# Kernel tuning notes

Hardware: AMD Instinct MI355X
Metric: run time of the kernel (lower is better)

The kernel has to match this reference:

```python
import jax, jax.numpy as jnp
import numpy as np

B, L, D, H = 1024, 128, 768, 256
EPS = 1e-5  # torch BatchNorm1d default eps


def _masked_mean(x, lens):
    # x: [B, L, D], lens: [B] int -> mean over first lens[i] rows per sample
    mask = (jnp.arange(x.shape[1])[None, :] < lens[:, None]).astype(x.dtype)  # [B, L]
    return jnp.einsum('bld,bl->bd', x, mask) / lens[:, None].astype(x.dtype)


def _batchnorm_train(x, gamma, beta):
    # training-mode BN: batch mean and biased variance
    mu = jnp.mean(x, axis=0)
    var = jnp.mean((x - mu) ** 2, axis=0)
    return gamma * (x - mu) / jnp.sqrt(var + EPS) + beta


def setup_inputs() -> dict:
    key = jax.random.key(0)
    ks = jax.random.split(key, 12)
    user_features = jax.random.normal(ks[0], (B, L, D), jnp.float32)
    hashtag_features = jax.random.normal(ks[1], (B, L, D), jnp.float32)
    user_lens = jax.random.randint(ks[2], (B,), 1, L + 1, jnp.int32)
    hashtag_lens = jax.random.randint(ks[3], (B,), 1, L + 1, jnp.int32)
    def lin(k, fan_out, fan_in):
        bound = 1.0 / np.sqrt(fan_in)
        kw, kb = jax.random.split(k)
        w = jax.random.uniform(kw, (fan_out, fan_in), jnp.float32, -bound, bound)
        b = jax.random.uniform(kb, (fan_out,), jnp.float32, -bound, bound)
        return w, b
    fc1_w, fc1_b = lin(ks[4], D, 2 * D)
    fc2_w, fc2_b = lin(ks[5], H, D)
    fc3_w, fc3_b = lin(ks[6], 1, H)
    bn1_g = jnp.ones((D,), jnp.float32)
    bn1_b = jnp.zeros((D,), jnp.float32)
    bn2_g = jnp.ones((H,), jnp.float32)
    bn2_b = jnp.zeros((H,), jnp.float32)
    return {
        'user_features': user_features, 'hashtag_features': hashtag_features,
        'user_lens': user_lens, 'hashtag_lens': hashtag_lens,
        'fc1_w': fc1_w, 'fc1_b': fc1_b, 'bn1_g': bn1_g, 'bn1_b': bn1_b,
        'fc2_w': fc2_w, 'fc2_b': fc2_b, 'bn2_g': bn2_g, 'bn2_b': bn2_b,
        'fc3_w': fc3_w, 'fc3_b': fc3_b,
    }


def reference(user_features, hashtag_features, user_lens, hashtag_lens,
              fc1_w, fc1_b, bn1_g, bn1_b, fc2_w, fc2_b, bn2_g, bn2_b,
              fc3_w, fc3_b):
    # fused ragged mean pooling (replaces per-sample python loop)
    u = _masked_mean(user_features, user_lens)       # [B, D]
    h = _masked_mean(hashtag_features, hashtag_lens)  # [B, D]
    x = jnp.concatenate([u, h], axis=1)               # [B, 2D]
    x = jax.nn.relu(_batchnorm_train(x @ fc1_w.T + fc1_b, bn1_g, bn1_b))
    x = jax.nn.relu(_batchnorm_train(x @ fc2_w.T + fc2_b, bn2_g, bn2_b))
    out = jax.nn.sigmoid(x @ fc3_w.T + fc3_b)          # [B, 1]
    return out
```

## Files before the change

kernel.cpp:

```cpp
#include <hip/hip_runtime.h>
#include <cstdint>
#include <cstddef>

#define BATCH 1024
#define SEQL  128
#define DIM   768
#define HID   256
#define KIN1  1536
#define BN_EPS 1e-5f

typedef unsigned short u16;
typedef __attribute__((ext_vector_type(8))) short short8;
typedef __attribute__((ext_vector_type(4))) float f32x4;

__device__ __forceinline__ u16 f2bf(float f) {
  uint32_t u = __float_as_uint(f);
  return (u16)((u + 0x7fffu + ((u >> 16) & 1u)) >> 16);
}
__device__ __forceinline__ f32x4 ntl(const f32x4* p) { return __builtin_nontemporal_load(p); }
__device__ __forceinline__ float kred(float v) {
  v += __shfl_xor(v, 16);
  v += __shfl_xor(v, 32);
  return v;
}

#define PREP_BLK 224
#define NW1Q (DIM * KIN1 / 4)
#define NWQ  (NW1Q + HID * DIM / 4)

__global__ __launch_bounds__(192) void pool_prep_kernel(
    const float* __restrict__ uf, const float* __restrict__ hf,
    const int* __restrict__ ul, const int* __restrict__ hl,
    const float* __restrict__ w1, const float* __restrict__ w2,
    u16* __restrict__ xb, u16* __restrict__ w1b, u16* __restrict__ w2b) {
  const int id = blockIdx.x;
  const int t = threadIdx.x;
  if (id < 2048) {
    const int b = id >> 1;
    const int which = id & 1;
    const f32x4* src = (const f32x4*)((which ? hf : uf) + (size_t)b * (SEQL * DIM));
    const int len = which ? hl[b] : ul[b];
    f32x4 a0 = (f32x4){0.f, 0.f, 0.f, 0.f}, a1 = a0, a2 = a0, a3 = a0;
    int l = 0;
    for (; l + 8 <= len; l += 8) {
      f32x4 v0 = ntl(src + (size_t)(l + 0) * 192 + t);
      f32x4 v1 = ntl(src + (size_t)(l + 1) * 192 + t);
      f32x4 v2 = ntl(src + (size_t)(l + 2) * 192 + t);
      f32x4 v3 = ntl(src + (size_t)(l + 3) * 192 + t);
      f32x4 v4 = ntl(src + (size_t)(l + 4) * 192 + t);
      f32x4 v5 = ntl(src + (size_t)(l + 5) * 192 + t);
      f32x4 v6 = ntl(src + (size_t)(l + 6) * 192 + t);
      f32x4 v7 = ntl(src + (size_t)(l + 7) * 192 + t);
      a0 += v0; a1 += v1; a2 += v2; a3 += v3;
      a0 += v4; a1 += v5; a2 += v6; a3 += v7;
    }
    for (; l < len; ++l) a0 += ntl(src + (size_t)l * 192 + t);
    a0 += a1; a2 += a3; a0 += a2;
    const float s = 1.f / (float)len;
    ushort4 o = make_ushort4(f2bf(a0[0] * s), f2bf(a0[1] * s), f2bf(a0[2] * s), f2bf(a0[3] * s));
    *(ushort4*)(xb + (size_t)b * KIN1 + which * DIM + t * 4) = o;
  } else {
    const int j = id - 2048;
    const int base = j * 192 + t;
#pragma unroll
    for (int s = 0; s < 8; ++s) {
      const int i = base + s * (PREP_BLK * 192);
      if (i < NW1Q) {
        f32x4 v = ((const f32x4*)w1)[i];
        ((ushort4*)w1b)[i] = make_ushort4(f2bf(v[0]), f2bf(v[1]), f2bf(v[2]), f2bf(v[3]));
      } else {
        const int i2 = i - NW1Q;
        f32x4 v = ((const f32x4*)w2)[i2];
        ((ushort4*)w2b)[i2] = make_ushort4(f2bf(v[0]), f2bf(v[1]), f2bf(v[2]), f2bf(v[3]));
      }
    }
  }
}

#define LDT 72

__global__ __launch_bounds__(256) void gemm1_kernel(
    const u16* __restrict__ A, const u16* __restrict__ W,
    const float* __restrict__ bias, float* __restrict__ y, float* __restrict__ p1) {
  __shared__ u16 lA[2][64 * LDT];
  __shared__ u16 lB[2][64 * LDT];
  __shared__ float red[2][64][2];
  const int K = KIN1, N = DIM;
  const int tid = threadIdx.x, lane = tid & 63, wv = tid >> 6;
  const int wr = wv >> 1, wc = wv & 1;
  const int r16 = lane & 15, kgrp = lane >> 4;
  const int d = blockIdx.x;
  const int g = d & 7, j = d >> 3;
  const int bm = (g >> 1) * 4 + (j & 3);
  const int bn = (g & 1) * 6 + (j >> 2);
  const int sr = tid >> 3, sc8 = (tid & 7) * 8;

  f32x4 acc[2][2];
#pragma unroll
  for (int mi = 0; mi < 2; ++mi)
#pragma unroll
    for (int ni = 0; ni < 2; ++ni) acc[mi][ni] = (f32x4){0.f, 0.f, 0.f, 0.f};

  const u16* Ab = A + (size_t)bm * 64 * K;
  const u16* Wb = W + (size_t)bn * 64 * K;

  uint4 ra0, ra1, rb0, rb1;
#define G1_LOAD(k0)                                              \
  ra0 = *(const uint4*)(Ab + (size_t)sr * K + (k0) + sc8);       \
  ra1 = *(const uint4*)(Ab + (size_t)(sr + 32) * K + (k0) + sc8);\
  rb0 = *(const uint4*)(Wb + (size_t)sr * K + (k0) + sc8);       \
  rb1 = *(const uint4*)(Wb + (size_t)(sr + 32) * K + (k0) + sc8);
#define G1_WRITE(buf)                                \
  *(uint4*)(lA[buf] + sr * LDT + sc8) = ra0;         \
  *(uint4*)(lA[buf] + (sr + 32) * LDT + sc8) = ra1;  \
  *(uint4*)(lB[buf] + sr * LDT + sc8) = rb0;         \
  *(uint4*)(lB[buf] + (sr + 32) * LDT + sc8) = rb1;

  G1_LOAD(0)
  G1_WRITE(0)
  __syncthreads();
  const int nk = K / 64;
  for (int ti = 0; ti < nk; ++ti) {
    const int cur = ti & 1;
    const bool more = (ti + 1 < nk);
    if (more) { G1_LOAD((ti + 1) * 64) }
#pragma unroll
    for (int kk = 0; kk < 2; ++kk) {
      const int koff = (kk * 4 + kgrp) * 8;
      short8 af0 = *(const short8*)(lA[cur] + (wr * 32 + r16) * LDT + koff);
      short8 af1 = *(const short8*)(lA[cur] + (wr * 32 + 16 + r16) * LDT + koff);
      short8 bf0 = *(const short8*)(lB[cur] + (wc * 32 + r16) * LDT + koff);
      short8 bf1 = *(const short8*)(lB[cur] + (wc * 32 + 16 + r16) * LDT + koff);
      acc[0][0] = __builtin_amdgcn_mfma_f32_16x16x32_bf16(af0, bf0, acc[0][0], 0, 0, 0);
      acc[0][1] = __builtin_amdgcn_mfma_f32_16x16x32_bf16(af0, bf1, acc[0][1], 0, 0, 0);
      acc[1][0] = __builtin_amdgcn_mfma_f32_16x16x32_bf16(af1, bf0, acc[1][0], 0, 0, 0);
      acc[1][1] = __builtin_amdgcn_mfma_f32_16x16x32_bf16(af1, bf1, acc[1][1], 0, 0, 0);
    }
    if (more) { G1_WRITE(cur ^ 1) }
    __syncthreads();
  }

#pragma unroll
  for (int ni = 0; ni < 2; ++ni) {
    const int col = bn * 64 + wc * 32 + ni * 16 + r16;
    const float bv = bias[col];
    float s = 0.f, s2 = 0.f;
#pragma unroll
    for (int mi = 0; mi < 2; ++mi)
#pragma unroll
      for (int rg = 0; rg < 4; ++rg) {
        const int row = bm * 64 + wr * 32 + mi * 16 + kgrp * 4 + rg;
        const float v = acc[mi][ni][rg] + bv;
        y[(size_t)row * N + col] = v;
        s += v; s2 += v * v;
      }
    s = kred(s); s2 = kred(s2);
    if (lane < 16) {
      red[wr][wc * 32 + ni * 16 + r16][0] = s;
      red[wr][wc * 32 + ni * 16 + r16][1] = s2;
    }
  }
  __syncthreads();
  if (tid < 128) {
    const int col = tid >> 1, wh = tid & 1;
    p1[((size_t)bm * DIM + bn * 64 + col) * 2 + wh] = red[0][col][wh] + red[1][col][wh];
  }
}

__global__ __launch_bounds__(256) void gemm2_kernel(
    const float* __restrict__ y1, const u16* __restrict__ W,
    const float* __restrict__ bias, const float* __restrict__ g, const float* __restrict__ be,
    const float* __restrict__ p1, float* __restrict__ y2, float* __restrict__ p2) {
  __shared__ u16 lA[2][32 * LDT];
  __shared__ u16 lB[2][32 * LDT];
  __shared__ float sS[DIM], sH[DIM];
  __shared__ float red[2][32][2];
  const int K = DIM, N = HID;
  const int tid = threadIdx.x, lane = tid & 63, wv = tid >> 6;
  const int wr = wv >> 1, wc = wv & 1;
  const int r16 = lane & 15, kgrp = lane >> 4;
  const int d = blockIdx.x;
  const int g8 = d & 7, j = d >> 3;
  const int bm = g8 * 4 + (j & 3);
  const int bn = j >> 2;
  const int sr = tid >> 3, sc8 = (tid & 7) * 8;

  for (int c = tid; c < DIM; c += 256) {
    float s = 0.f, s2 = 0.f;
#pragma unroll
    for (int i = 0; i < 16; ++i) {
      float2 pv = *(const float2*)(p1 + ((size_t)i * DIM + c) * 2);
      s += pv.x; s2 += pv.y;
    }
    const float m = s * (1.f / BATCH);
    const float var = s2 * (1.f / BATCH) - m * m;
    const float r = rsqrtf(var + BN_EPS);
    const float scl = r * g[c];
    sS[c] = scl;
    sH[c] = be[c] - m * scl;
  }
  __syncthreads();

  f32x4 acc = (f32x4){0.f, 0.f, 0.f, 0.f};
  const float* Ab = y1 + (size_t)bm * 32 * K;
  const u16* Wb = W + (size_t)bn * 32 * K;

  f32x4 va0, va1;
  uint4 rbq;
#define G2_LOAD(k0)                                          \
  va0 = *(const f32x4*)(Ab + (size_t)sr * K + (k0) + sc8);   \
  va1 = *(const f32x4*)(Ab + (size_t)sr * K + (k0) + sc8 + 4);\
  rbq = *(const uint4*)(Wb + (size_t)sr * K + (k0) + sc8);

  auto pack_write = [&](int buf, int k0) {
    union { ushort us[8]; uint4 q; } pk;
#pragma unroll
    for (int jj = 0; jj < 4; ++jj) {
      pk.us[jj]     = f2bf(fmaxf(0.f, va0[jj] * sS[k0 + sc8 + jj] + sH[k0 + sc8 + jj]));
      pk.us[4 + jj] = f2bf(fmaxf(0.f, va1[jj] * sS[k0 + sc8 + 4 + jj] + sH[k0 + sc8 + 4 + jj]));
    }
    *(uint4*)(lA[buf] + sr * LDT + sc8) = pk.q;
    *(uint4*)(lB[buf] + sr * LDT + sc8) = rbq;
  };

  G2_LOAD(0)
  pack_write(0, 0);
  __syncthreads();
  const int nk = K / 64;
  for (int ti = 0; ti < nk; ++ti) {
    const int cur = ti & 1;
    const bool more = (ti + 1 < nk);
    if (more) { G2_LOAD((ti + 1) * 64) }
#pragma unroll
    for (int kk = 0; kk < 2; ++kk) {
      const int koff = (kk * 4 + kgrp) * 8;
      short8 af0 = *(const short8*)(lA[cur] + (wr * 16 + r16) * LDT + koff);
      short8 bf0 = *(const short8*)(lB[cur] + (wc * 16 + r16) * LDT + koff);
      acc = __builtin_amdgcn_mfma_f32_16x16x32_bf16(af0, bf0, acc, 0, 0, 0);
    }
    if (more) pack_write(cur ^ 1, (ti + 1) * 64);
    __syncthreads();
  }

  {
    const int col = bn * 32 + wc * 16 + r16;
    const float bv = bias[col];
    float s = 0.f, s2 = 0.f;
#pragma unroll
    for (int rg = 0; rg < 4; ++rg) {
      const int row = bm * 32 + wr * 16 + kgrp * 4 + rg;
      const float v = acc[rg] + bv;
      y2[(size_t)row * N + col] = v;
      s += v; s2 += v * v;
    }
    s = kred(s); s2 = kred(s2);
    if (lane < 16) {
      red[wr][wc * 16 + r16][0] = s;
      red[wr][wc * 16 + r16][1] = s2;
    }
  }
  __syncthreads();
  if (tid < 64) {
    const int col = tid >> 1, wh = tid & 1;
    p2[((size_t)bm * HID + bn * 32 + col) * 2 + wh] = red[0][col][wh] + red[1][col][wh];
  }
}

__global__ __launch_bounds__(256) void fc3_kernel(
    const float* __restrict__ y2, const float* __restrict__ p2,
    const float* __restrict__ g, const float* __restrict__ be,
    const float* __restrict__ w3, const float* __restrict__ b3, float* __restrict__ out) {
  __shared__ float sS[HID], sH[HID];
  const int tid = threadIdx.x;
  {
    const int c = tid;
    float s = 0.f, s2 = 0.f;
#pragma unroll
    for (int i = 0; i < 32; ++i) {
      float2 pv = *(const float2*)(p2 + ((size_t)i * HID + c) * 2);
      s += pv.x; s2 += pv.y;
    }
    const float m = s * (1.f / BATCH);
    const float var = s2 * (1.f / BATCH) - m * m;
    const float r = rsqrtf(var + BN_EPS);
    const float scl = r * g[c];
    sS[c] = scl;
    sH[c] = be[c] - m * scl;
  }
  __syncthreads();
  const int row = blockIdx.x * 4 + (tid >> 6);
  const int lane = tid & 63;
  f32x4 xv = *(const f32x4*)(y2 + (size_t)row * HID + lane * 4);
  f32x4 sc = *(const f32x4*)&sS[lane * 4];
  f32x4 sh = *(const f32x4*)&sH[lane * 4];
  f32x4 wv = *(const f32x4*)(w3 + lane * 4);
  float dsum = 0.f;
#pragma unroll
  for (int jj = 0; jj < 4; ++jj) dsum += fmaxf(0.f, xv[jj] * sc[jj] + sh[jj]) * wv[jj];
#pragma unroll
  for (int off = 32; off > 0; off >>= 1) dsum += __shfl_xor(dsum, off);
  if (lane == 0) out[row] = 1.f / (1.f + expf(-(dsum + b3[0])));
}

extern "C" void kernel_launch(void* const* d_in, const int* in_sizes, int n_in,
                              void* d_out, int out_size, void* d_ws, size_t ws_size,
                              hipStream_t stream) {
  const float* uf   = (const float*)d_in[0];
  const float* hf   = (const float*)d_in[1];
  const int*   ul   = (const int*)d_in[2];
  const int*   hl   = (const int*)d_in[3];
  const float* fc1w = (const float*)d_in[4];
  const float* fc1b = (const float*)d_in[5];
  const float* bn1g = (const float*)d_in[6];
  const float* bn1b = (const float*)d_in[7];
  const float* fc2w = (const float*)d_in[8];
  const float* fc2b = (const float*)d_in[9];
  const float* bn2g = (const float*)d_in[10];
  const float* bn2b = (const float*)d_in[11];
  const float* fc3w = (const float*)d_in[12];
  const float* fc3b = (const float*)d_in[13];
  float* out = (float*)d_out;

  char* ws = (char*)d_ws;
  u16*   xb  = (u16*)  (ws + 0);
  u16*   w1b = (u16*)  (ws + 3145728);
  u16*   w2b = (u16*)  (ws + 5505024);
  float* y1  = (float*)(ws + 5898240);
  float* y2  = (float*)(ws + 9043968);
  float* p1  = (float*)(ws + 10092544);
  float* p2  = (float*)(ws + 10190848);

  pool_prep_kernel<<<2048 + PREP_BLK, 192, 0, stream>>>(uf, hf, ul, hl, fc1w, fc2w, xb, w1b, w2b);
  gemm1_kernel<<<192, 256, 0, stream>>>(xb, w1b, fc1b, y1, p1);
  gemm2_kernel<<<256, 256, 0, stream>>>(y1, w2b, fc2b, bn1g, bn1b, p1, y2, p2);
  fc3_kernel<<<256, 256, 0, stream>>>(y2, p2, bn2g, bn2b, fc3w, fc3b, out);
}
```

Before: 112.5 us.

## Fuse GEMM1, GEMM2 and FC3 into one persistent kernel with grid barriers

Merges the three post-pooling kernels into a single 256-block kernel that uses atomic-counter grid barriers between the stages, which removes two kernel launch gaps. It also reorders the prep kernel so the weight-conversion blocks are scheduled first, and switches the pooling loads from nontemporal to regular loads. The cost is a memset launch for the counters, spin-wait barriers that rely on all 256 blocks being co-resident, and 64 blocks sitting idle during GEMM1.

```diff
diff --git a/kernel.cpp b/kernel.cpp
--- a/kernel.cpp
+++ b/kernel.cpp
@@ -17,7 +17,6 @@
   uint32_t u = __float_as_uint(f);
   return (u16)((u + 0x7fffu + ((u >> 16) & 1u)) >> 16);
 }
-__device__ __forceinline__ f32x4 ntl(const f32x4* p) { return __builtin_nontemporal_load(p); }
 __device__ __forceinline__ float kred(float v) {
   v += __shfl_xor(v, 16);
   v += __shfl_xor(v, 32);
@@ -35,32 +34,33 @@
     u16* __restrict__ xb, u16* __restrict__ w1b, u16* __restrict__ w2b) {
   const int id = blockIdx.x;
   const int t = threadIdx.x;
-  if (id < 2048) {
-    const int b = id >> 1;
-    const int which = id & 1;
+  if (id >= PREP_BLK) {
+    const int job = id - PREP_BLK;
+    const int b = job >> 1;
+    const int which = job & 1;
     const f32x4* src = (const f32x4*)((which ? hf : uf) + (size_t)b * (SEQL * DIM));
     const int len = which ? hl[b] : ul[b];
     f32x4 a0 = (f32x4){0.f, 0.f, 0.f, 0.f}, a1 = a0, a2 = a0, a3 = a0;
     int l = 0;
     for (; l + 8 <= len; l += 8) {
-      f32x4 v0 = ntl(src + (size_t)(l + 0) * 192 + t);
-      f32x4 v1 = ntl(src + (size_t)(l + 1) * 192 + t);
-      f32x4 v2 = ntl(src + (size_t)(l + 2) * 192 + t);
-      f32x4 v3 = ntl(src + (size_t)(l + 3) * 192 + t);
-      f32x4 v4 = ntl(src + (size_t)(l + 4) * 192 + t);
-      f32x4 v5 = ntl(src + (size_t)(l + 5) * 192 + t);
-      f32x4 v6 = ntl(src + (size_t)(l + 6) * 192 + t);
-      f32x4 v7 = ntl(src + (size_t)(l + 7) * 192 + t);
+      f32x4 v0 = src[(size_t)(l + 0) * 192 + t];
+      f32x4 v1 = src[(size_t)(l + 1) * 192 + t];
+      f32x4 v2 = src[(size_t)(l + 2) * 192 + t];
+      f32x4 v3 = src[(size_t)(l + 3) * 192 + t];
+      f32x4 v4 = src[(size_t)(l + 4) * 192 + t];
+      f32x4 v5 = src[(size_t)(l + 5) * 192 + t];
+      f32x4 v6 = src[(size_t)(l + 6) * 192 + t];
+      f32x4 v7 = src[(size_t)(l + 7) * 192 + t];
       a0 += v0; a1 += v1; a2 += v2; a3 += v3;
       a0 += v4; a1 += v5; a2 += v6; a3 += v7;
     }
-    for (; l < len; ++l) a0 += ntl(src + (size_t)l * 192 + t);
+    for (; l < len; ++l) a0 += src[(size_t)l * 192 + t];
     a0 += a1; a2 += a3; a0 += a2;
     const float s = 1.f / (float)len;
     ushort4 o = make_ushort4(f2bf(a0[0] * s), f2bf(a0[1] * s), f2bf(a0[2] * s), f2bf(a0[3] * s));
     *(ushort4*)(xb + (size_t)b * KIN1 + which * DIM + t * 4) = o;
   } else {
-    const int j = id - 2048;
+    const int j = id;
     const int base = j * 192 + t;
 #pragma unroll
     for (int s = 0; s < 8; ++s) {
@@ -79,227 +79,248 @@
 
 #define LDT 72
 
-__global__ __launch_bounds__(256) void gemm1_kernel(
-    const u16* __restrict__ A, const u16* __restrict__ W,
-    const float* __restrict__ bias, float* __restrict__ y, float* __restrict__ p1) {
-  __shared__ u16 lA[2][64 * LDT];
-  __shared__ u16 lB[2][64 * LDT];
-  __shared__ float red[2][64][2];
-  const int K = KIN1, N = DIM;
+__device__ __forceinline__ void grid_barrier(unsigned* cnt, unsigned nblk) {
+  __syncthreads();
+  if (threadIdx.x == 0) {
+    __threadfence();
+    atomicAdd(cnt, 1u);
+    while (__hip_atomic_load(cnt, __ATOMIC_RELAXED, __HIP_MEMORY_SCOPE_AGENT) < nblk)
+      __builtin_amdgcn_s_sleep(2);
+    __threadfence();
+  }
+  __syncthreads();
+}
+
+__global__ __launch_bounds__(256, 1) void fused_tail_kernel(
+    const u16* __restrict__ A, const u16* __restrict__ W1,
+    const u16* __restrict__ W2,
+    const float* __restrict__ b1, const float* __restrict__ g1v, const float* __restrict__ be1,
+    const float* __restrict__ b2, const float* __restrict__ g2v, const float* __restrict__ be2,
+    const float* __restrict__ w3, const float* __restrict__ b3,
+    float* __restrict__ y1, float* __restrict__ p1,
+    float* __restrict__ y2, float* __restrict__ p2,
+    unsigned* __restrict__ cnt, float* __restrict__ out) {
+  __shared__ alignas(16) char smem[38912];
   const int tid = threadIdx.x, lane = tid & 63, wv = tid >> 6;
   const int wr = wv >> 1, wc = wv & 1;
   const int r16 = lane & 15, kgrp = lane >> 4;
-  const int d = blockIdx.x;
-  const int g = d & 7, j = d >> 3;
-  const int bm = (g >> 1) * 4 + (j & 3);
-  const int bn = (g & 1) * 6 + (j >> 2);
   const int sr = tid >> 3, sc8 = (tid & 7) * 8;
 
-  f32x4 acc[2][2];
-#pragma unroll
-  for (int mi = 0; mi < 2; ++mi)
-#pragma unroll
-    for (int ni = 0; ni < 2; ++ni) acc[mi][ni] = (f32x4){0.f, 0.f, 0.f, 0.f};
-
-  const u16* Ab = A + (size_t)bm * 64 * K;
-  const u16* Wb = W + (size_t)bn * 64 * K;
-
-  uint4 ra0, ra1, rb0, rb1;
+  if (blockIdx.x < 192) {
+    u16* lA = (u16*)smem;
+    u16* lB = (u16*)(smem + 18432);
+    float (*red)[64][2] = (float(*)[64][2])(smem + 36864);
+    const int K = KIN1, N = DIM;
+    const int d = blockIdx.x;
+    const int g = d & 7, j = d >> 3;
+    const int bm = (g >> 1) * 4 + (j & 3);
+    const int bn = (g & 1) * 6 + (j >> 2);
+
+    f32x4 acc[2][2];
+#pragma unroll
+    for (int mi = 0; mi < 2; ++mi)
+#pragma unroll
+      for (int ni = 0; ni < 2; ++ni) acc[mi][ni] = (f32x4){0.f, 0.f, 0.f, 0.f};
+
+    const u16* Ab = A + (size_t)bm * 64 * K;
+    const u16* Wb = W1 + (size_t)bn * 64 * K;
+
+    uint4 ra0, ra1, rb0, rb1;
 #define G1_LOAD(k0)                                              \
   ra0 = *(const uint4*)(Ab + (size_t)sr * K + (k0) + sc8);       \
   ra1 = *(const uint4*)(Ab + (size_t)(sr + 32) * K + (k0) + sc8);\
   rb0 = *(const uint4*)(Wb + (size_t)sr * K + (k0) + sc8);       \
   rb1 = *(const uint4*)(Wb + (size_t)(sr + 32) * K + (k0) + sc8);
-#define G1_WRITE(buf)                                \
-  *(uint4*)(lA[buf] + sr * LDT + sc8) = ra0;         \
-  *(uint4*)(lA[buf] + (sr + 32) * LDT + sc8) = ra1;  \
-  *(uint4*)(lB[buf] + sr * LDT + sc8) = rb0;         \
-  *(uint4*)(lB[buf] + (sr + 32) * LDT + sc8) = rb1;
-
-  G1_LOAD(0)
-  G1_WRITE(0)
-  __syncthreads();
-  const int nk = K / 64;
-  for (int ti = 0; ti < nk; ++ti) {
-    const int cur = ti & 1;
-    const bool more = (ti + 1 < nk);
-    if (more) { G1_LOAD((ti + 1) * 64) }
-#pragma unroll
-    for (int kk = 0; kk < 2; ++kk) {
-      const int koff = (kk * 4 + kgrp) * 8;
-      short8 af0 = *(const short8*)(lA[cur] + (wr * 32 + r16) * LDT + koff);
-      short8 af1 = *(const short8*)(lA[cur] + (wr * 32 + 16 + r16) * LDT + koff);
-      short8 bf0 = *(const short8*)(lB[cur] + (wc * 32 + r16) * LDT + koff);
-      short8 bf1 = *(const short8*)(lB[cur] + (wc * 32 + 16 + r16) * LDT + koff);
-      acc[0][0] = __builtin_amdgcn_mfma_f32_16x16x32_bf16(af0, bf0, acc[0][0], 0, 0, 0);
-      acc[0][1] = __builtin_amdgcn_mfma_f32_16x16x32_bf16(af0, bf1, acc[0][1], 0, 0, 0);
-      acc[1][0] = __builtin_amdgcn_mfma_f32_16x16x32_bf16(af1, bf0, acc[1][0], 0, 0, 0);
-      acc[1][1] = __builtin_amdgcn_mfma_f32_16x16x32_bf16(af1, bf1, acc[1][1], 0, 0, 0);
-    }
-    if (more) { G1_WRITE(cur ^ 1) }
-    __syncthreads();
-  }
-
-#pragma unroll
-  for (int ni = 0; ni < 2; ++ni) {
-    const int col = bn * 64 + wc * 32 + ni * 16 + r16;
-    const float bv = bias[col];
-    float s = 0.f, s2 = 0.f;
-#pragma unroll
-    for (int mi = 0; mi < 2; ++mi)
-#pragma unroll
-      for (int rg = 0; rg < 4; ++rg) {
-        const int row = bm * 64 + wr * 32 + mi * 16 + kgrp * 4 + rg;
-        const float v = acc[mi][ni][rg] + bv;
-        y[(size_t)row * N + col] = v;
-        s += v; s2 += v * v;
-      }
-    s = kred(s); s2 = kred(s2);
-    if (lane < 16) {
-      red[wr][wc * 32 + ni * 16 + r16][0] = s;
-      red[wr][wc * 32 + ni * 16 + r16][1] = s2;
-    }
-  }
-  __syncthreads();
-  if (tid < 128) {
-    const int col = tid >> 1, wh = tid & 1;
-    p1[((size_t)bm * DIM + bn * 64 + col) * 2 + wh] = red[0][col][wh] + red[1][col][wh];
-  }
-}
-
-__global__ __launch_bounds__(256) void gemm2_kernel(
-    const float* __restrict__ y1, const u16* __restrict__ W,
-    const float* __restrict__ bias, const float* __restrict__ g, const float* __restrict__ be,
-    const float* __restrict__ p1, float* __restrict__ y2, float* __restrict__ p2) {
-  __shared__ u16 lA[2][32 * LDT];
-  __shared__ u16 lB[2][32 * LDT];
-  __shared__ float sS[DIM], sH[DIM];
-  __shared__ float red[2][32][2];
-  const int K = DIM, N = HID;
-  const int tid = threadIdx.x, lane = tid & 63, wv = tid >> 6;
-  const int wr = wv >> 1, wc = wv & 1;
-  const int r16 = lane & 15, kgrp = lane >> 4;
-  const int d = blockIdx.x;
-  const int g8 = d & 7, j = d >> 3;
-  const int bm = g8 * 4 + (j & 3);
-  const int bn = j >> 2;
-  const int sr = tid >> 3, sc8 = (tid & 7) * 8;
-
-  for (int c = tid; c < DIM; c += 256) {
-    float s = 0.f, s2 = 0.f;
-#pragma unroll
-    for (int i = 0; i < 16; ++i) {
-      float2 pv = *(const float2*)(p1 + ((size_t)i * DIM + c) * 2);
-      s += pv.x; s2 += pv.y;
-    }
-    const float m = s * (1.f / BATCH);
-    const float var = s2 * (1.f / BATCH) - m * m;
-    const float r = rsqrtf(var + BN_EPS);
-    const float scl = r * g[c];
-    sS[c] = scl;
-    sH[c] = be[c] - m * scl;
-  }
-  __syncthreads();
-
-  f32x4 acc = (f32x4){0.f, 0.f, 0.f, 0.f};
-  const float* Ab = y1 + (size_t)bm * 32 * K;
-  const u16* Wb = W + (size_t)bn * 32 * K;
-
-  f32x4 va0, va1;
-  uint4 rbq;
-#define G2_LOAD(k0)                                          \
-  va0 = *(const f32x4*)(Ab + (size_t)sr * K + (k0) + sc8);   \
+#define G1_WRITE(buf)                                            \
+  *(uint4*)(lA + (buf) * (64 * LDT) + sr * LDT + sc8) = ra0;     \
+  *(uint4*)(lA + (buf) * (64 * LDT) + (sr + 32) * LDT + sc8) = ra1; \
+  *(uint4*)(lB + (buf) * (64 * LDT) + sr * LDT + sc8) = rb0;     \
+  *(uint4*)(lB + (buf) * (64 * LDT) + (sr + 32) * LDT + sc8) = rb1;
+
+    G1_LOAD(0)
+    G1_WRITE(0)
+    __syncthreads();
+    const int nk = K / 64;
+    for (int ti = 0; ti < nk; ++ti) {
+      const int cur = ti & 1;
+      const bool more = (ti + 1 < nk);
+      if (more) { G1_LOAD((ti + 1) * 64) }
+#pragma unroll
+      for (int kk = 0; kk < 2; ++kk) {
+        const int koff = (kk * 4 + kgrp) * 8;
+        const u16* lac = lA + cur * (64 * LDT);
+        const u16* lbc = lB + cur * (64 * LDT);
+        short8 af0 = *(const short8*)(lac + (wr * 32 + r16) * LDT + koff);
+        short8 af1 = *(const short8*)(lac + (wr * 32 + 16 + r16) * LDT + koff);
+        short8 bf0 = *(const short8*)(lbc + (wc * 32 + r16) * LDT + koff);
+        short8 bf1 = *(const short8*)(lbc + (wc * 32 + 16 + r16) * LDT + koff);
+        acc[0][0] = __builtin_amdgcn_mfma_f32_16x16x32_bf16(af0, bf0, acc[0][0], 0, 0, 0);
+        acc[0][1] = __builtin_amdgcn_mfma_f32_16x16x32_bf16(af0, bf1, acc[0][1], 0, 0, 0);
+        acc[1][0] = __builtin_amdgcn_mfma_f32_16x16x32_bf16(af1, bf0, acc[1][0], 0, 0, 0);
+        acc[1][1] = __builtin_amdgcn_mfma_f32_16x16x32_bf16(af1, bf1, acc[1][1], 0, 0, 0);
+      }
+      if (more) { G1_WRITE(cur ^ 1) }
+      __syncthreads();
+    }
+#undef G1_LOAD
+#undef G1_WRITE
+
+#pragma unroll
+    for (int ni = 0; ni < 2; ++ni) {
+      const int col = bn * 64 + wc * 32 + ni * 16 + r16;
+      const float bv = b1[col];
+      float s = 0.f, s2 = 0.f;
+#pragma unroll
+      for (int mi = 0; mi < 2; ++mi)
+#pragma unroll
+        for (int rg = 0; rg < 4; ++rg) {
+          const int row = bm * 64 + wr * 32 + mi * 16 + kgrp * 4 + rg;
+          const float v = acc[mi][ni][rg] + bv;
+          y1[(size_t)row * N + col] = v;
+          s += v; s2 += v * v;
+        }
+      s = kred(s); s2 = kred(s2);
+      if (lane < 16) {
+        red[wr][wc * 32 + ni * 16 + r16][0] = s;
+        red[wr][wc * 32 + ni * 16 + r16][1] = s2;
+      }
+    }
+    __syncthreads();
+    if (tid < 128) {
+      const int col = tid >> 1, wh = tid & 1;
+      p1[((size_t)bm * DIM + bn * 64 + col) * 2 + wh] = red[0][col][wh] + red[1][col][wh];
+    }
+  }
+
+  grid_barrier(cnt, 256);
+
+  {
+    u16* lA = (u16*)smem;
+    u16* lB = (u16*)(smem + 9216);
+    float* sS = (float*)(smem + 18432);
+    float* sH = (float*)(smem + 21504);
+    float (*red)[32][2] = (float(*)[32][2])(smem + 24576);
+    const int K = DIM, N = HID;
+    const int d = blockIdx.x;
+    const int g8 = d & 7, j = d >> 3;
+    const int bm = g8 * 4 + (j & 3);
+    const int bn = j >> 2;
+
+    for (int c = tid; c < DIM; c += 256) {
+      float s = 0.f, s2 = 0.f;
+#pragma unroll
+      for (int i = 0; i < 16; ++i) {
+        float2 pv = *(const float2*)(p1 + ((size_t)i * DIM + c) * 2);
+        s += pv.x; s2 += pv.y;
+      }
+      const float m = s * (1.f / BATCH);
+      const float var = s2 * (1.f / BATCH) - m * m;
+      const float r = rsqrtf(var + BN_EPS);
+      const float scl = r * g1v[c];
+      sS[c] = scl;
+      sH[c] = be1[c] - m * scl;
+    }
+    __syncthreads();
+
+    f32x4 acc = (f32x4){0.f, 0.f, 0.f, 0.f};
+    const float* Ab = y1 + (size_t)bm * 32 * K;
+    const u16* Wb = W2 + (size_t)bn * 32 * K;
+
+    f32x4 va0, va1;
+    uint4 rbq;
+#define G2_LOAD(k0)                                           \
+  va0 = *(const f32x4*)(Ab + (size_t)sr * K + (k0) + sc8);    \
   va1 = *(const f32x4*)(Ab + (size_t)sr * K + (k0) + sc8 + 4);\
   rbq = *(const uint4*)(Wb + (size_t)sr * K + (k0) + sc8);
 
-  auto pack_write = [&](int buf, int k0) {
-    union { ushort us[8]; uint4 q; } pk;
-#pragma unroll
-    for (int jj = 0; jj < 4; ++jj) {
-      pk.us[jj]     = f2bf(fmaxf(0.f, va0[jj] * sS[k0 + sc8 + jj] + sH[k0 + sc8 + jj]));
-      pk.us[4 + jj] = f2bf(fmaxf(0.f, va1[jj] * sS[k0 + sc8 + 4 + jj] + sH[k0 + sc8 + 4 + jj]));
-    }
-    *(uint4*)(lA[buf] + sr * LDT + sc8) = pk.q;
-    *(uint4*)(lB[buf] + sr * LDT + sc8) = rbq;
-  };
-
-  G2_LOAD(0)
-  pack_write(0, 0);
-  __syncthreads();
-  const int nk = K / 64;
-  for (int ti = 0; ti < nk; ++ti) {
-    const int cur = ti & 1;
-    const bool more = (ti + 1 < nk);
-    if (more) { G2_LOAD((ti + 1) * 64) }
-#pragma unroll
-    for (int kk = 0; kk < 2; ++kk) {
-      const int koff = (kk * 4 + kgrp) * 8;
-      short8 af0 = *(const short8*)(lA[cur] + (wr * 16 + r16) * LDT + koff);
-      short8 bf0 = *(const short8*)(lB[cur] + (wc * 16 + r16) * LDT + koff);
-      acc = __builtin_amdgcn_mfma_f32_16x16x32_bf16(af0, bf0, acc, 0, 0, 0);
-    }
-    if (more) pack_write(cur ^ 1, (ti + 1) * 64);
-    __syncthreads();
-  }
+    auto pack_write = [&](int buf, int k0) {
+      union { ushort us[8]; uint4 q; } pk;
+#pragma unroll
+      for (int jj = 0; jj < 4; ++jj) {
+        pk.us[jj]     = f2bf(fmaxf(0.f, va0[jj] * sS[k0 + sc8 + jj] + sH[k0 + sc8 + jj]));
+        pk.us[4 + jj] = f2bf(fmaxf(0.f, va1[jj] * sS[k0 + sc8 + 4 + jj] + sH[k0 + sc8 + 4 + jj]));
+      }
+      *(uint4*)(lA + buf * (32 * LDT) + sr * LDT + sc8) = pk.q;
+      *(uint4*)(lB + buf * (32 * LDT) + sr * LDT + sc8) = rbq;
+    };
+
+    G2_LOAD(0)
+    pack_write(0, 0);
+    __syncthreads();
+    const int nk = K / 64;
+    for (int ti = 0; ti < nk; ++ti) {
+      const int cur = ti & 1;
+      const bool more = (ti + 1 < nk);
+      if (more) { G2_LOAD((ti + 1) * 64) }
+#pragma unroll
+      for (int kk = 0; kk < 2; ++kk) {
+        const int koff = (kk * 4 + kgrp) * 8;
+        short8 af0 = *(const short8*)(lA + cur * (32 * LDT) + (wr * 16 + r16) * LDT + koff);
+        short8 bf0 = *(const short8*)(lB + cur * (32 * LDT) + (wc * 16 + r16) * LDT + koff);
+        acc = __builtin_amdgcn_mfma_f32_16x16x32_bf16(af0, bf0, acc, 0, 0, 0);
+      }
+      if (more) pack_write(cur ^ 1, (ti + 1) * 64);
+      __syncthreads();
+    }
+#undef G2_LOAD
+
+    {
+      const int col = bn * 32 + wc * 16 + r16;
+      const float bv = b2[col];
+      float s = 0.f, s2 = 0.f;
+#pragma unroll
+      for (int rg = 0; rg < 4; ++rg) {
+        const int row = bm * 32 + wr * 16 + kgrp * 4 + rg;
+        const float v = acc[rg] + bv;
+        y2[(size_t)row * N + col] = v;
+        s += v; s2 += v * v;
+      }
+      s = kred(s); s2 = kred(s2);
+      if (lane < 16) {
+        red[wr][wc * 16 + r16][0] = s;
+        red[wr][wc * 16 + r16][1] = s2;
+      }
+    }
+    __syncthreads();
+    if (tid < 64) {
+      const int col = tid >> 1, wh = tid & 1;
+      p2[((size_t)bm * HID + bn * 32 + col) * 2 + wh] = red[0][col][wh] + red[1][col][wh];
+    }
+  }
+
+  grid_barrier(cnt + 1, 256);
 
   {
-    const int col = bn * 32 + wc * 16 + r16;
-    const float bv = bias[col];
-    float s = 0.f, s2 = 0.f;
-#pragma unroll
-    for (int rg = 0; rg < 4; ++rg) {
-      const int row = bm * 32 + wr * 16 + kgrp * 4 + rg;
-      const float v = acc[rg] + bv;
-      y2[(size_t)row * N + col] = v;
-      s += v; s2 += v * v;
-    }
-    s = kred(s); s2 = kred(s2);
-    if (lane < 16) {
-      red[wr][wc * 16 + r16][0] = s;
-      red[wr][wc * 16 + r16][1] = s2;
-    }
-  }
-  __syncthreads();
-  if (tid < 64) {
-    const int col = tid >> 1, wh = tid & 1;
-    p2[((size_t)bm * HID + bn * 32 + col) * 2 + wh] = red[0][col][wh] + red[1][col][wh];
-  }
-}
-
-__global__ __launch_bounds__(256) void fc3_kernel(
-    const float* __restrict__ y2, const float* __restrict__ p2,
-    const float* __restrict__ g, const float* __restrict__ be,
-    const float* __restrict__ w3, const float* __restrict__ b3, float* __restrict__ out) {
-  __shared__ float sS[HID], sH[HID];
-  const int tid = threadIdx.x;
-  {
-    const int c = tid;
-    float s = 0.f, s2 = 0.f;
-#pragma unroll
-    for (int i = 0; i < 32; ++i) {
-      float2 pv = *(const float2*)(p2 + ((size_t)i * HID + c) * 2);
-      s += pv.x; s2 += pv.y;
-    }
-    const float m = s * (1.f / BATCH);
-    const float var = s2 * (1.f / BATCH) - m * m;
-    const float r = rsqrtf(var + BN_EPS);
-    const float scl = r * g[c];
-    sS[c] = scl;
-    sH[c] = be[c] - m * scl;
-  }
-  __syncthreads();
-  const int row = blockIdx.x * 4 + (tid >> 6);
-  const int lane = tid & 63;
-  f32x4 xv = *(const f32x4*)(y2 + (size_t)row * HID + lane * 4);
-  f32x4 sc = *(const f32x4*)&sS[lane * 4];
-  f32x4 sh = *(const f32x4*)&sH[lane * 4];
-  f32x4 wv = *(const f32x4*)(w3 + lane * 4);
-  float dsum = 0.f;
-#pragma unroll
-  for (int jj = 0; jj < 4; ++jj) dsum += fmaxf(0.f, xv[jj] * sc[jj] + sh[jj]) * wv[jj];
-#pragma unroll
-  for (int off = 32; off > 0; off >>= 1) dsum += __shfl_xor(dsum, off);
-  if (lane == 0) out[row] = 1.f / (1.f + expf(-(dsum + b3[0])));
+    float* sS = (float*)smem;
+    float* sH = (float*)(smem + 1024);
+    {
+      const int c = tid;
+      float s = 0.f, s2 = 0.f;
+#pragma unroll
+      for (int i = 0; i < 32; ++i) {
+        float2 pv = *(const float2*)(p2 + ((size_t)i * HID + c) * 2);
+        s += pv.x; s2 += pv.y;
+      }
+      const float m = s * (1.f / BATCH);
+      const float var = s2 * (1.f / BATCH) - m * m;
+      const float r = rsqrtf(var + BN_EPS);
+      const float scl = r * g2v[c];
+      sS[c] = scl;
+      sH[c] = be2[c] - m * scl;
+    }
+    __syncthreads();
+    const int row = blockIdx.x * 4 + (tid >> 6);
+    f32x4 xv = *(const f32x4*)(y2 + (size_t)row * HID + lane * 4);
+    f32x4 sc = *(const f32x4*)&sS[lane * 4];
+    f32x4 sh = *(const f32x4*)&sH[lane * 4];
+    f32x4 wv = *(const f32x4*)(w3 + lane * 4);
+    float dsum = 0.f;
+#pragma unroll
+    for (int jj = 0; jj < 4; ++jj) dsum += fmaxf(0.f, xv[jj] * sc[jj] + sh[jj]) * wv[jj];
+#pragma unroll
+    for (int off = 32; off > 0; off >>= 1) dsum += __shfl_xor(dsum, off);
+    if (lane == 0) out[row] = 1.f / (1.f + expf(-(dsum + b3[0])));
+  }
 }
 
 extern "C" void kernel_launch(void* const* d_in, const int* in_sizes, int n_in,
@@ -329,9 +350,11 @@
   float* y2  = (float*)(ws + 9043968);
   float* p1  = (float*)(ws + 10092544);
   float* p2  = (float*)(ws + 10190848);
-
-  pool_prep_kernel<<<2048 + PREP_BLK, 192, 0, stream>>>(uf, hf, ul, hl, fc1w, fc2w, xb, w1b, w2b);
-  gemm1_kernel<<<192, 256, 0, stream>>>(xb, w1b, fc1b, y1, p1);
-  gemm2_kernel<<<256, 256, 0, stream>>>(y1, w2b, fc2b, bn1g, bn1b, p1, y2, p2);
-  fc3_kernel<<<256, 256, 0, stream>>>(y2, p2, bn2g, bn2b, fc3w, fc3b, out);
-}
+  unsigned* cnt = (unsigned*)(ws + 10256384);
+
+  hipMemsetAsync(cnt, 0, 8, stream);
+  pool_prep_kernel<<<PREP_BLK + 2048, 192, 0, stream>>>(uf, hf, ul, hl, fc1w, fc2w, xb, w1b, w2b);
+  fused_tail_kernel<<<256, 256, 0, stream>>>(xb, w1b, w2b, fc1b, bn1g, bn1b,
+                                             fc2b, bn2g, bn2b, fc3w, fc3b,
+                                             y1, p1, y2, p2, cnt, out);
+}
```

Measured after the change: 171.4 us. 1.52x slower.
